# Performance work log

Measured on AMD Instinct MI355X. Metric: run time of the kernel, lower is better.

The kernel has to match this reference:

```python
import jax, jax.numpy as jnp
import numpy as np

B, N, C, H = 16, 577, 768, 12
KEEP_RATE = 0.7


def setup_inputs() -> dict:
    key = jax.random.key(0)
    k1, k2, k3 = jax.random.split(key, 3)
    x = jax.random.normal(k1, (B, N, C), dtype=jnp.float32)
    W_qkv = jax.random.normal(k2, (C, 3 * C), dtype=jnp.float32) * 0.02
    W_proj = jax.random.normal(k3, (C, C), dtype=jnp.float32) * 0.02
    b_proj = jnp.zeros((C,), dtype=jnp.float32)
    return {"x": x, "W_qkv": W_qkv, "W_proj": W_proj, "b_proj": b_proj}


def reference(x, W_qkv, W_proj, b_proj):
    b, n, c = x.shape
    h = H
    dh = c // h
    scale = dh ** (-0.5)

    # qkv projection -> q,k,v each [B,H,N,dh]
    qkv = (x @ W_qkv).reshape(b, n, 3, h, dh)
    qkv = jnp.transpose(qkv, (2, 0, 3, 1, 4))
    q, k, v = qkv[0], qkv[1], qkv[2]

    # full attention scores [B,H,N,N] (materialized, as in the source)
    attn = jnp.einsum('bhnd,bhmd->bhnm', q, k) * scale

    # --- top_pool from row-0 (CLS) scores, attn_method == 'SUM_ABS_1' ---
    # attn[:, :, 0, :] -> [B,H,N]; sum |.| over heads -> [B,N] (== mean over C=1 channel)
    attn_weight = jnp.sum(jnp.abs(attn[:, :, 0, :]), axis=1)  # [B,N]
    # exclude_first=True: drop CLS, topk over remaining N-1, alpha1=1, alpha2=0 (C==1 -> std=0)
    w = attn_weight[:, 1:]                       # [B, N-1]
    keep_num = max(int((n - 1) * KEEP_RATE), 1)  # static
    _, idx = jax.lax.top_k(w, keep_num)          # [B, keep_num]
    idx = jnp.sort(idx, axis=1)
    idx = jnp.concatenate(
        [jnp.zeros((b, 1), dtype=idx.dtype), idx + 1], axis=1)  # prepend CLS index 0
    # expand to [B, keep_num+1, dim] as in torch (pool dim kwarg == self.dim)
    keep_index = jnp.broadcast_to(idx[:, :, None], (b, keep_num + 1, c))

    # standard attention output
    a = jax.nn.softmax(attn, axis=-1)
    out = jnp.einsum('bhnm,bhmd->bhnd', a, v)    # [B,H,N,dh]
    out = jnp.transpose(out, (0, 2, 1, 3)).reshape(b, n, c)
    out = out @ W_proj + b_proj
    return out, keep_index
```

## Files before the change

### kernel.cpp

```cpp
#include <hip/hip_runtime.h>
#include <hip/hip_bf16.h>
#include <stdint.h>

#define B_    16
#define N_    577
#define C_    768
#define H_    12
#define M_    (B_*N_)
#define QKVN  (3*C_)
#define NKEEP 403
#define KROWS (NKEEP+1)
#define VTLD  640
#define PTLD  72

typedef short s16x8 __attribute__((ext_vector_type(8)));
typedef float f32x4 __attribute__((ext_vector_type(4)));

__device__ __forceinline__ unsigned short f2bf(float x){
  unsigned int u = __float_as_uint(x);
  u += 0x7FFF + ((u >> 16) & 1);
  return (unsigned short)(u >> 16);
}

__device__ __forceinline__ void gld_lds16(const void* g, void* l){
  __builtin_amdgcn_global_load_lds(
      (const __attribute__((address_space(1))) unsigned int*)g,
      (__attribute__((address_space(3))) unsigned int*)l, 16, 0, 0);
}

template<int NT, int M9, int MTILES>
__device__ __forceinline__ void tile_map(int L, int& mt, int& nt){
  constexpr int NB = MTILES*NT;
  int x = L & 7, j = L >> 3;
  if(j < M9*NT){
    nt = j/M9; mt = x*M9 + (j - nt*M9);
  } else {
    int offt = 0;
    #pragma unroll
    for(int y=0;y<8;y++) if(y<x) offt += ((NB-1-y)>>3) + 1 - M9*NT;
    int ft = offt + (j - M9*NT);
    mt = 8*M9 + ft/NT;
    nt = ft - (ft/NT)*NT;
  }
}

__global__ void k_cvt_x(const float* __restrict__ x, unsigned short* __restrict__ xb){
  int i = blockIdx.x*256 + threadIdx.x;
  float4 v = ((const float4*)x)[i];
  ushort4 o; o.x=f2bf(v.x); o.y=f2bf(v.y); o.z=f2bf(v.z); o.w=f2bf(v.w);
  ((ushort4*)xb)[i] = o;
}

__global__ void k_transpose_cvt(const float* __restrict__ in, unsigned short* __restrict__ out,
                                int R, int CC){
  __shared__ float tile[64][65];
  int r0 = blockIdx.y*64, c0 = blockIdx.x*64;
  int tx = threadIdx.x & 63, ty = threadIdx.x >> 6;
  #pragma unroll
  for(int i=0;i<16;i++){
    int r = ty + i*4;
    tile[r][tx] = in[(size_t)(r0+r)*CC + c0 + tx];
  }
  __syncthreads();
  #pragma unroll
  for(int i=0;i<16;i++){
    int c = ty + i*4;
    out[(size_t)(c0+c)*R + r0 + tx] = f2bf(tile[tx][c]);
  }
}

template<int LDC_, bool BF16OUT, bool FUSEV, int NT>
__global__ __launch_bounds__(256) void k_gemm_bt(const unsigned short* __restrict__ A,
                          const unsigned short* __restrict__ Bt,
                          void* __restrict__ Cout,
                          const float* __restrict__ bias, int Mdim,
                          unsigned short* __restrict__ vtbuf){
  __shared__ __align__(16) unsigned short As[128*32];
  __shared__ __align__(16) unsigned short Bs[128*32];
  const int t = threadIdx.x;
  const int w = t>>6, l = t&63, lq = l>>4, lr = l&15;
  const int wm = w>>1, wn = w&1;
  int mt, nt; tile_map<NT, 9, 73>(blockIdx.x, mt, nt);
  const int m0 = mt*128, n0 = nt*128;
  int rA0 = m0 + (t>>2);       if(rA0 >= Mdim) rA0 = Mdim-1;
  int rA1 = m0 + ((t+256)>>2); if(rA1 >= Mdim) rA1 = Mdim-1;
  const unsigned short* gA0 = A  + (size_t)rA0*768 + (t&3)*8;
  const unsigned short* gA1 = A  + (size_t)rA1*768 + (t&3)*8;
  const unsigned short* gB0 = Bt + (size_t)(n0 + (t>>2))*768 + (t&3)*8;
  const unsigned short* gB1 = Bt + (size_t)(n0 + ((t+256)>>2))*768 + (t&3)*8;
  unsigned short* lA0 = As + (size_t)w*512;
  unsigned short* lA1 = As + 2048 + (size_t)w*512;
  unsigned short* lB0 = Bs + (size_t)w*512;
  unsigned short* lB1 = Bs + 2048 + (size_t)w*512;
  f32x4 acc[4][4] = {};
  for(int kt=0; kt<24; ++kt){
    const int ko = kt*32;
    __syncthreads();
    gld_lds16(gA0 + ko, lA0); gld_lds16(gA1 + ko, lA1);
    gld_lds16(gB0 + ko, lB0); gld_lds16(gB1 + ko, lB1);
    __syncthreads();
    s16x8 af[4], bfr[4];
    #pragma unroll
    for(int it=0;it<4;it++) af[it]  = *(const s16x8*)&As[(wm*64+it*16+lr)*32 + lq*8];
    #pragma unroll
    for(int jt=0;jt<4;jt++) bfr[jt] = *(const s16x8*)&Bs[(wn*64+jt*16+lr)*32 + lq*8];
    #pragma unroll
    for(int it=0;it<4;it++)
      #pragma unroll
      for(int jt=0;jt<4;jt++)
        acc[it][jt] = __builtin_amdgcn_mfma_f32_16x16x32_bf16(af[it], bfr[jt], acc[it][jt], 0,0,0);
  }
  if(FUSEV && n0 >= 1536){
    #pragma unroll
    for(int it=0;it<4;it++){
      int tok0 = m0 + wm*64 + it*16 + lq*4;
      #pragma unroll
      for(int jt=0;jt<4;jt++){
        int vrow = (n0 - 1536) + wn*64 + jt*16 + lr;
        ushort4 pk; unsigned short* pks = (unsigned short*)&pk;
        #pragma unroll
        for(int r=0;r<4;r++) pks[r] = f2bf(acc[it][jt][r]);
        int b0 = tok0/577, t0 = tok0 - b0*577;
        if(tok0 + 3 < M_ && t0 + 3 < 577){
          *(ushort4*)&vtbuf[(size_t)(b0*768 + vrow)*VTLD + t0] = pk;
        } else {
          #pragma unroll
          for(int r=0;r<4;r++){
            int tg = tok0 + r;
            if(tg < M_){
              int bb = tg/577, tt = tg - bb*577;
              vtbuf[(size_t)(bb*768 + vrow)*VTLD + tt] = pks[r];
            }
          }
        }
      }
    }
  } else {
    #pragma unroll
    for(int it=0;it<4;it++){
      #pragma unroll
      for(int r=0;r<4;r++){
        int row = m0 + wm*64 + it*16 + lq*4 + r;
        if(row < Mdim){
          #pragma unroll
          for(int jt=0;jt<4;jt++){
            int col = n0 + wn*64 + jt*16 + lr;
            float v = acc[it][jt][r];
            if constexpr (BF16OUT)
              ((unsigned short*)Cout)[(size_t)row*LDC_ + col] = f2bf(v);
            else
              ((float*)Cout)[(size_t)row*LDC_ + col] = v + bias[col];
          }
        }
      }
    }
  }
}

__global__ __launch_bounds__(256) void k_gemm_bt64(const unsigned short* __restrict__ A,
                          const unsigned short* __restrict__ Bt,
                          float* __restrict__ Cout,
                          const float* __restrict__ bias, int Mdim){
  __shared__ __align__(16) unsigned short As[64*32];
  __shared__ __align__(16) unsigned short Bs[128*32];
  const int t = threadIdx.x;
  const int w = t>>6, l = t&63, lq = l>>4, lr = l&15;
  const int wm = w>>1, wn = w&1;
  int mt, nt; tile_map<6, 18, 145>(blockIdx.x, mt, nt);
  const int m0 = mt*64, n0 = nt*128;
  int rA0 = m0 + (t>>2);       if(rA0 >= Mdim) rA0 = Mdim-1;
  const unsigned short* gA0 = A  + (size_t)rA0*768 + (t&3)*8;
  const unsigned short* gB0 = Bt + (size_t)(n0 + (t>>2))*768 + (t&3)*8;
  const unsigned short* gB1 = Bt + (size_t)(n0 + ((t+256)>>2))*768 + (t&3)*8;
  unsigned short* lA0 = As + (size_t)w*512;
  unsigned short* lB0 = Bs + (size_t)w*512;
  unsigned short* lB1 = Bs + 2048 + (size_t)w*512;
  f32x4 acc[2][4] = {};
  for(int kt=0; kt<24; ++kt){
    const int ko = kt*32;
    __syncthreads();
    gld_lds16(gA0 + ko, lA0);
    gld_lds16(gB0 + ko, lB0); gld_lds16(gB1 + ko, lB1);
    __syncthreads();
    s16x8 af[2], bfr[4];
    #pragma unroll
    for(int it=0;it<2;it++) af[it]  = *(const s16x8*)&As[(wm*32+it*16+lr)*32 + lq*8];
    #pragma unroll
    for(int jt=0;jt<4;jt++) bfr[jt] = *(const s16x8*)&Bs[(wn*64+jt*16+lr)*32 + lq*8];
    #pragma unroll
    for(int it=0;it<2;it++)
      #pragma unroll
      for(int jt=0;jt<4;jt++)
        acc[it][jt] = __builtin_amdgcn_mfma_f32_16x16x32_bf16(af[it], bfr[jt], acc[it][jt], 0,0,0);
  }
  #pragma unroll
  for(int it=0;it<2;it++){
    #pragma unroll
    for(int r=0;r<4;r++){
      int row = m0 + wm*32 + it*16 + lq*4 + r;
      if(row < Mdim){
        #pragma unroll
        for(int jt=0;jt<4;jt++){
          int col = n0 + wn*64 + jt*16 + lr;
          Cout[(size_t)row*768 + col] = acc[it][jt][r] + bias[col];
        }
      }
    }
  }
}

__global__ __launch_bounds__(256,4) void k_attn(const unsigned short* __restrict__ qkv,
                                                const unsigned short* __restrict__ vtbuf,
                                                unsigned short* __restrict__ aout){
  __shared__ __align__(16) unsigned short Ks[64*64];
  __shared__ __align__(16) unsigned short Vt[64*64];
  __shared__ __align__(16) unsigned short Ptt[128*PTLD];
  __shared__ float Ls[4][2][16][4];
  const int blk = blockIdx.x;
  const int bh = blk % 192, qt = blk / 192;
  const int b = bh / 12, h = bh % 12;
  const int t = threadIdx.x, w = t>>6, l = t&63, lq = l>>4, lr = l&15;
  const size_t base = (size_t)(b*577)*2304 + h*64;
  const int q0 = qt*128;
  s16x8 bq[2][2];
  #pragma unroll
  for(int it=0;it<2;it++){
    int qrow = q0 + w*32 + it*16 + lr; if(qrow > 576) qrow = 576;
    #pragma unroll
    for(int ks=0;ks<2;ks++)
      bq[it][ks] = *(const s16x8*)&qkv[base + (size_t)qrow*2304 + ks*32 + lq*8];
  }
  const int srow = w*8 + (l>>3);
  const int cswz8 = (((l&7) ^ (l>>3)) << 3);
  unsigned short* ldsK = Ks + (size_t)w*512;
  unsigned short* ldsV = Vt + (size_t)w*512;
  const unsigned short* gVbase = vtbuf + (size_t)(bh*64)*VTLD + cswz8;

  f32x4 acc_o[2][4] = {};
  float lsum[2] = {0.f, 0.f};
  const float CEXP = 0.18033688011112043f;

  auto tile_body = [&](int j0, bool edge){
    __syncthreads();
    #pragma unroll
    for(int i=0;i<2;i++){
      int krow = j0 + i*32 + srow; if(krow > 576) krow = 576;
      gld_lds16(qkv + base + 768 + (size_t)krow*2304 + cswz8, ldsK + i*2048);
      gld_lds16(gVbase + (size_t)(i*32 + srow)*VTLD + j0,     ldsV + i*2048);
    }
    __syncthreads();
    f32x4 accs[2][4] = {};
    #pragma unroll
    for(int ks=0;ks<2;ks++){
      s16x8 ak[4];
      #pragma unroll
      for(int jt=0;jt<4;jt++){
        int j = jt*16 + lr;
        ak[jt] = *(const s16x8*)&Ks[j*64 + (((4*ks+lq) ^ (j&7))<<3)];
      }
      #pragma unroll
      for(int it=0;it<2;it++)
        #pragma unroll
        for(int jt=0;jt<4;jt++)
          accs[it][jt] = __builtin_amdgcn_mfma_f32_16x16x32_bf16(ak[jt], bq[it][ks], accs[it][jt], 0,0,0);
    }
    #pragma unroll
    for(int it=0;it<2;it++){
      int qlocal = w*32 + it*16 + lr;
      #pragma unroll
      for(int jt=0;jt<4;jt++){
        ushort4 pk;
        unsigned short* pks = (unsigned short*)&pk;
        #pragma unroll
        for(int r=0;r<4;r++){
          float p = exp2f(accs[it][jt][r] * CEXP);
          if(edge){ if(j0 + jt*16 + lq*4 + r > 576) p = 0.f; }
          lsum[it] += p;
          pks[r] = f2bf(p);
        }
        *(ushort4*)&Ptt[qlocal*PTLD + jt*16 + lq*4] = pk;
      }
    }
    #pragma unroll
    for(int ks=0;ks<2;ks++){
      s16x8 ap[2], bv[4];
      #pragma unroll
      for(int it=0;it<2;it++)
        ap[it] = *(const s16x8*)&Ptt[(w*32+it*16+lr)*PTLD + ks*32 + lq*8];
      #pragma unroll
      for(int dt=0;dt<4;dt++){
        int d = dt*16 + lr;
        bv[dt] = *(const s16x8*)&Vt[d*64 + (((4*ks+lq) ^ (d&7))<<3)];
      }
      #pragma unroll
      for(int it=0;it<2;it++)
        #pragma unroll
        for(int dt=0;dt<4;dt++)
          acc_o[it][dt] = __builtin_amdgcn_mfma_f32_16x16x32_bf16(ap[it], bv[dt], acc_o[it][dt], 0,0,0);
    }
  };
  for(int j0=0; j0<576; j0+=64) tile_body(j0, false);
  tile_body(576, true);

  #pragma unroll
  for(int it=0;it<2;it++) Ls[w][it][lr][lq] = lsum[it];
  #pragma unroll
  for(int it=0;it<2;it++){
    #pragma unroll
    for(int r=0;r<4;r++){
      int n = q0 + w*32 + it*16 + lq*4 + r;
      if(n <= 576){
        int q16 = lq*4 + r;
        float lt = Ls[w][it][q16][0] + Ls[w][it][q16][1] + Ls[w][it][q16][2] + Ls[w][it][q16][3];
        float inv = 1.f / lt;
        #pragma unroll
        for(int dt=0;dt<4;dt++)
          aout[(size_t)(b*577+n)*768 + h*64 + dt*16 + lr] = f2bf(acc_o[it][dt][r]*inv);
      }
    }
  }
}

__global__ void k_qcls(const float* __restrict__ x, const float* __restrict__ Wqkv,
                       float* __restrict__ qcls){
  __shared__ float xs[768];
  __shared__ float part[4][64];
  const int b = blockIdx.y, j0 = blockIdx.x*64;
  const int t = threadIdx.x;
  const float* xr = x + (size_t)b*577*768;
  xs[t] = xr[t]; xs[t+256] = xr[t+256]; xs[t+512] = xr[t+512];
  __syncthreads();
  const int jl = t & 63, cs = t >> 6;
  float acc = 0.f;
  const float* wp = Wqkv + (size_t)(cs*192)*2304 + j0 + jl;
  #pragma unroll 4
  for(int c=0;c<192;c++){ acc += xs[cs*192+c] * wp[0]; wp += 2304; }
  part[cs][jl] = acc;
  __syncthreads();
  if(t < 64) qcls[b*768 + j0 + t] = part[0][t]+part[1][t]+part[2][t]+part[3][t];
}
__global__ void k_u(const float* __restrict__ Wqkv, const float* __restrict__ qcls,
                    float* __restrict__ u){
  int h = blockIdx.x, b = blockIdx.y, c = threadIdx.x;
  const float* qc = qcls + b*768 + h*64;
  const float* wr = Wqkv + (size_t)c*2304 + 768 + h*64;
  float acc = 0.f;
  #pragma unroll
  for(int d=0;d<64;d++) acc += wr[d]*qc[d];
  u[(size_t)(b*12+h)*768 + c] = acc;
}
__global__ void k_attw(const float* __restrict__ x, const float* __restrict__ u,
                       float* __restrict__ attw){
  int blk = blockIdx.x;
  int b = blk/577, m = blk%577;
  int lane = threadIdx.x;
  const float* xr = x + (size_t)(b*577+m)*768;
  const float* ub = u + (size_t)b*12*768;
  float part[12];
  #pragma unroll
  for(int h=0;h<12;h++) part[h]=0.f;
  #pragma unroll
  for(int i=0;i<12;i++){
    float xv = xr[i*64 + lane];
    #pragma unroll
    for(int h=0;h<12;h++) part[h] += xv * ub[h*768 + i*64 + lane];
  }
  float s = 0.f;
  #pragma unroll
  for(int h=0;h<12;h++){
    float v = part[h];
    #pragma unroll
    for(int off=32; off; off>>=1) v += __shfl_xor(v, off);
    s += fabsf(v);
  }
  if(lane==0) attw[b*577 + m] = 0.125f * s;
}
__global__ void k_topk(const float* __restrict__ attw, int* __restrict__ idxbuf){
  __shared__ float sw[576];
  __shared__ int wtot[9];
  int b = blockIdx.x, t = threadIdx.x;
  float wv = attw[b*577 + 1 + t];
  sw[t] = wv;
  __syncthreads();
  int rank = 0;
  for(int j=0;j<576;j++){
    float wj = sw[j];
    rank += (wj > wv) || (wj == wv && j < t);
  }
  bool kept = rank < NKEEP;
  unsigned long long mask = __ballot(kept);
  int wid = t>>6, lane = t&63;
  int pos = __popcll(mask & ((1ull<<lane)-1ull));
  if(lane==0) wtot[wid] = __popcll(mask);
  __syncthreads();
  int off0 = 0;
  for(int q=0;q<wid;q++) off0 += wtot[q];
  if(kept) idxbuf[b*KROWS + 1 + off0 + pos] = t+1;
  if(t==0) idxbuf[b*KROWS] = 0;
}
__global__ void k_fill_keep(const int* __restrict__ idxbuf, float* __restrict__ out2){
  int i4 = blockIdx.x*256 + threadIdx.x;
  float v = (float)idxbuf[i4/192];
  ((float4*)out2)[i4] = make_float4(v,v,v,v);
}

extern "C" void kernel_launch(void* const* d_in, const int* in_sizes, int n_in,
                              void* d_out, int out_size, void* d_ws, size_t ws_size,
                              hipStream_t stream){
  const float* x     = (const float*)d_in[0];
  const float* Wqkv  = (const float*)d_in[1];
  const float* Wproj = (const float*)d_in[2];
  const float* bias  = (const float*)d_in[3];
  float* out  = (float*)d_out;
  float* out2 = out + (size_t)M_*768;

  char* ws = (char*)d_ws;
  size_t off = 0;
  auto alloc = [&](size_t bytes)->void*{ void* p = ws + off; off += (bytes + 255) & ~(size_t)255; return p; };
  unsigned short* xb     = (unsigned short*)alloc((size_t)M_*768*2);
  unsigned short* wqkvT  = (unsigned short*)alloc((size_t)QKVN*768*2);
  unsigned short* wprojT = (unsigned short*)alloc((size_t)768*768*2);
  unsigned short* qkvb   = (unsigned short*)alloc((size_t)M_*QKVN*2);
  unsigned short* aoutb  = (unsigned short*)alloc((size_t)M_*768*2);
  unsigned short* vtbuf  = (unsigned short*)alloc((size_t)192*64*VTLD*2);
  float* qcls   = (float*)alloc((size_t)16*768*4);
  float* u      = (float*)alloc((size_t)16*12*768*4);
  float* attw   = (float*)alloc((size_t)16*577*4);
  int*   idxbuf = (int*)alloc((size_t)16*KROWS*4);

  k_cvt_x<<<6924, 256, 0, stream>>>(x, xb);
  k_transpose_cvt<<<dim3(36,12), 256, 0, stream>>>(Wqkv,  wqkvT, 768, 2304);
  k_transpose_cvt<<<dim3(12,12), 256, 0, stream>>>(Wproj, wprojT, 768, 768);
  k_gemm_bt<QKVN, true, true, 18><<<73*18, 256, 0, stream>>>(xb, wqkvT, qkvb, nullptr, M_, vtbuf);
  k_qcls<<<dim3(12,16), 256, 0, stream>>>(x, Wqkv, qcls);
  k_u<<<dim3(12,16), 768, 0, stream>>>(Wqkv, qcls, u);
  k_attw<<<16*577, 64, 0, stream>>>(x, u, attw);
  k_topk<<<16, 576, 0, stream>>>(attw, idxbuf);
  k_fill_keep<<<(16*KROWS*768/4 + 255)/256, 256, 0, stream>>>(idxbuf, out2);
  k_attn<<<960, 256, 0, stream>>>(qkvb, vtbuf, aoutb);
  k_gemm_bt64<<<145*6, 256, 0, stream>>>(aoutb, wprojT, out, bias, M_);
}
```

Before: 282.8 us.

## Rewrite QKV GEMM as 256x256 tile with pipelined LDS double buffering

```diff
diff --git a/kernel.cpp b/kernel.cpp
--- a/kernel.cpp
+++ b/kernel.cpp
@@ -69,59 +69,135 @@
   }
 }
 
-template<int LDC_, bool BF16OUT, bool FUSEV, int NT>
-__global__ __launch_bounds__(256) void k_gemm_bt(const unsigned short* __restrict__ A,
+__global__ __launch_bounds__(512,2) void k_gemm_qkv(const unsigned short* __restrict__ A,
                           const unsigned short* __restrict__ Bt,
-                          void* __restrict__ Cout,
-                          const float* __restrict__ bias, int Mdim,
+                          unsigned short* __restrict__ qkvb,
                           unsigned short* __restrict__ vtbuf){
-  __shared__ __align__(16) unsigned short As[128*32];
-  __shared__ __align__(16) unsigned short Bs[128*32];
+  __shared__ __align__(16) unsigned short L[8][8192];
   const int t = threadIdx.x;
   const int w = t>>6, l = t&63, lq = l>>4, lr = l&15;
-  const int wm = w>>1, wn = w&1;
-  int mt, nt; tile_map<NT, 9, 73>(blockIdx.x, mt, nt);
-  const int m0 = mt*128, n0 = nt*128;
-  int rA0 = m0 + (t>>2);       if(rA0 >= Mdim) rA0 = Mdim-1;
-  int rA1 = m0 + ((t+256)>>2); if(rA1 >= Mdim) rA1 = Mdim-1;
-  const unsigned short* gA0 = A  + (size_t)rA0*768 + (t&3)*8;
-  const unsigned short* gA1 = A  + (size_t)rA1*768 + (t&3)*8;
-  const unsigned short* gB0 = Bt + (size_t)(n0 + (t>>2))*768 + (t&3)*8;
-  const unsigned short* gB1 = Bt + (size_t)(n0 + ((t+256)>>2))*768 + (t&3)*8;
-  unsigned short* lA0 = As + (size_t)w*512;
-  unsigned short* lA1 = As + 2048 + (size_t)w*512;
-  unsigned short* lB0 = Bs + (size_t)w*512;
-  unsigned short* lB1 = Bs + 2048 + (size_t)w*512;
-  f32x4 acc[4][4] = {};
-  for(int kt=0; kt<24; ++kt){
-    const int ko = kt*32;
-    __syncthreads();
-    gld_lds16(gA0 + ko, lA0); gld_lds16(gA1 + ko, lA1);
-    gld_lds16(gB0 + ko, lB0); gld_lds16(gB1 + ko, lB1);
-    __syncthreads();
-    s16x8 af[4], bfr[4];
-    #pragma unroll
-    for(int it=0;it<4;it++) af[it]  = *(const s16x8*)&As[(wm*64+it*16+lr)*32 + lq*8];
-    #pragma unroll
-    for(int jt=0;jt<4;jt++) bfr[jt] = *(const s16x8*)&Bs[(wn*64+jt*16+lr)*32 + lq*8];
-    #pragma unroll
-    for(int it=0;it<4;it++)
-      #pragma unroll
-      for(int jt=0;jt<4;jt++)
-        acc[it][jt] = __builtin_amdgcn_mfma_f32_16x16x32_bf16(af[it], bfr[jt], acc[it][jt], 0,0,0);
-  }
-  if(FUSEV && n0 >= 1536){
-    #pragma unroll
-    for(int it=0;it<4;it++){
-      int tok0 = m0 + wm*64 + it*16 + lq*4;
-      #pragma unroll
-      for(int jt=0;jt<4;jt++){
-        int vrow = (n0 - 1536) + wn*64 + jt*16 + lr;
+  const int wm = w>>2, wn = w&3;
+
+  int orig = blockIdx.x;
+  int xid = orig & 7, j = orig >> 3;
+  int wgid = (xid < 5 ? xid*42 : 210 + (xid-5)*41) + j;
+  int mt = wgid/9, nt = wgid - mt*9;
+  const int m0 = mt*256, n0 = nt*256;
+
+  const int rr = w*8 + (l>>3);
+  const int csw = ((l&7)*8) ^ ((l&32)?16:0);
+  int ra0 = m0 + rr;        if(ra0 >= M_) ra0 = M_-1;
+  int ra1 = m0 + 64 + rr;   if(ra1 >= M_) ra1 = M_-1;
+  int ra2 = m0 + 128 + rr;  if(ra2 >= M_) ra2 = M_-1;
+  int ra3 = m0 + 192 + rr;  if(ra3 >= M_) ra3 = M_-1;
+  const unsigned short* pA00 = A + (size_t)ra0*768 + csw;
+  const unsigned short* pA01 = A + (size_t)ra1*768 + csw;
+  const unsigned short* pA10 = A + (size_t)ra2*768 + csw;
+  const unsigned short* pA11 = A + (size_t)ra3*768 + csw;
+  const unsigned short* pB00 = Bt + (size_t)(n0 + rr)*768 + csw;
+  const unsigned short* pB01 = Bt + (size_t)(n0 + 64 + rr)*768 + csw;
+  const unsigned short* pB10 = Bt + (size_t)(n0 + 128 + rr)*768 + csw;
+  const unsigned short* pB11 = Bt + (size_t)(n0 + 192 + rr)*768 + csw;
+
+#define STAGE_A(H, KT, SLT) do{ \
+  unsigned short* d_ = &L[((H)<<1)|(SLT)][(w*8)<<6]; \
+  gld_lds16(pA##H##0 + (size_t)(KT)*64, d_); \
+  gld_lds16(pA##H##1 + (size_t)(KT)*64, d_ + 4096); \
+}while(0)
+#define STAGE_B(H, KT, SLT) do{ \
+  unsigned short* d_ = &L[4 + (((H)<<1)|(SLT))][(w*8)<<6]; \
+  gld_lds16(pB##H##0 + (size_t)(KT)*64, d_); \
+  gld_lds16(pB##H##1 + (size_t)(KT)*64, d_ + 4096); \
+}while(0)
+#define READ_A(MH) do{ \
+  _Pragma("unroll") \
+  for(int mf=0; mf<4; mf++){ \
+    const int R_ = (MH)*64 + mf*16 + lr; \
+    const int rx_ = (R_&4)<<2; \
+    af[mf][0] = *(const s16x8*)&baseA[R_*64 + ((lq*8) ^ rx_)]; \
+    af[mf][1] = *(const s16x8*)&baseA[R_*64 + ((32 + lq*8) ^ rx_)]; \
+  } \
+}while(0)
+#define READ_B() do{ \
+  _Pragma("unroll") \
+  for(int nf=0; nf<4; nf++){ \
+    const int R_ = (wn&1)*64 + nf*16 + lr; \
+    const int rx_ = (R_&4)<<2; \
+    bf[nf][0] = *(const s16x8*)&baseB[R_*64 + ((lq*8) ^ rx_)]; \
+    bf[nf][1] = *(const s16x8*)&baseB[R_*64 + ((32 + lq*8) ^ rx_)]; \
+  } \
+}while(0)
+#define MMA_Q(MH, NH) do{ \
+  __builtin_amdgcn_s_setprio(1); \
+  _Pragma("unroll") \
+  for(int ks=0; ks<2; ks++){ \
+    _Pragma("unroll") \
+    for(int mf=0; mf<4; mf++){ \
+      _Pragma("unroll") \
+      for(int nf=0; nf<2; nf++){ \
+        acc[(MH)*4+mf][(NH)*2+nf] = __builtin_amdgcn_mfma_f32_16x16x32_bf16( \
+            af[mf][ks], bf[(NH)*2+nf][ks], acc[(MH)*4+mf][(NH)*2+nf], 0,0,0); \
+      } } } \
+  __builtin_amdgcn_s_setprio(0); \
+}while(0)
+
+  f32x4 acc[8][4] = {};
+  s16x8 af[4][2], bf[4][2];
+  const unsigned short* baseA0 = &L[wm<<1][0];
+  const unsigned short* baseB0 = &L[4 + ((wn>>1)<<1)][0];
+
+  STAGE_A(0, 0, 0); STAGE_A(1, 0, 0); STAGE_B(0, 0, 0); STAGE_B(1, 0, 0);
+  STAGE_B(0, 1, 1); STAGE_B(1, 1, 1); STAGE_A(0, 1, 1);
+  asm volatile("s_waitcnt vmcnt(6)" ::: "memory");
+  __builtin_amdgcn_s_barrier();
+
+  for(int g=0; g<12; ++g){
+    const int s = g&1;
+    const unsigned short* baseA = baseA0 + (s<<13);
+    const unsigned short* baseB = baseB0 + (s<<13);
+    READ_A(0);
+    READ_B();
+    if(g<11){ STAGE_A(1, g+1, s^1); }
+    __builtin_amdgcn_s_barrier();
+    asm volatile("s_waitcnt lgkmcnt(0)" ::: "memory");
+    __builtin_amdgcn_sched_barrier(0);
+    MMA_Q(0,0);
+    __builtin_amdgcn_s_barrier();
+    if(g<10){ STAGE_B(0, g+2, s); }
+    __builtin_amdgcn_s_barrier();
+    MMA_Q(0,1);
+    __builtin_amdgcn_s_barrier();
+    READ_A(1);
+    if(g<10){ STAGE_B(1, g+2, s); }
+    __builtin_amdgcn_s_barrier();
+    asm volatile("s_waitcnt lgkmcnt(0)" ::: "memory");
+    __builtin_amdgcn_sched_barrier(0);
+    MMA_Q(1,1);
+    __builtin_amdgcn_s_barrier();
+    if(g<10){
+      STAGE_A(0, g+2, s);
+      asm volatile("s_waitcnt vmcnt(6)" ::: "memory");
+    } else if(g==10){
+      asm volatile("s_waitcnt vmcnt(0)" ::: "memory");
+    }
+    __builtin_amdgcn_s_barrier();
+    MMA_Q(1,0);
+    __builtin_amdgcn_s_barrier();
+  }
+
+  if(n0 >= 1536){
+    #pragma unroll
+    for(int mi=0; mi<8; mi++){
+      int tok0 = m0 + wm*128 + mi*16 + lq*4;
+      int b0 = tok0/577, t0 = tok0 - b0*577;
+      bool fast = (tok0 + 3 < M_) && (t0 + 3 < 577);
+      #pragma unroll
+      for(int ni=0; ni<4; ni++){
+        int vrow = (n0 - 1536) + wn*64 + ni*16 + lr;
         ushort4 pk; unsigned short* pks = (unsigned short*)&pk;
         #pragma unroll
-        for(int r=0;r<4;r++) pks[r] = f2bf(acc[it][jt][r]);
-        int b0 = tok0/577, t0 = tok0 - b0*577;
-        if(tok0 + 3 < M_ && t0 + 3 < 577){
+        for(int r=0;r<4;r++) pks[r] = f2bf(acc[mi][ni][r]);
+        if(fast){
           *(ushort4*)&vtbuf[(size_t)(b0*768 + vrow)*VTLD + t0] = pk;
         } else {
           #pragma unroll
@@ -137,24 +213,25 @@
     }
   } else {
     #pragma unroll
-    for(int it=0;it<4;it++){
+    for(int mi=0; mi<8; mi++){
       #pragma unroll
       for(int r=0;r<4;r++){
-        int row = m0 + wm*64 + it*16 + lq*4 + r;
-        if(row < Mdim){
+        int row = m0 + wm*128 + mi*16 + lq*4 + r;
+        if(row < M_){
           #pragma unroll
-          for(int jt=0;jt<4;jt++){
-            int col = n0 + wn*64 + jt*16 + lr;
-            float v = acc[it][jt][r];
-            if constexpr (BF16OUT)
-              ((unsigned short*)Cout)[(size_t)row*LDC_ + col] = f2bf(v);
-            else
-              ((float*)Cout)[(size_t)row*LDC_ + col] = v + bias[col];
+          for(int ni=0; ni<4; ni++){
+            int col = n0 + wn*64 + ni*16 + lr;
+            qkvb[(size_t)row*2304 + col] = f2bf(acc[mi][ni][r]);
           }
         }
       }
     }
   }
+#undef STAGE_A
+#undef STAGE_B
+#undef READ_A
+#undef READ_B
+#undef MMA_Q
 }
 
 __global__ __launch_bounds__(256) void k_gemm_bt64(const unsigned short* __restrict__ A,
@@ -431,7 +508,7 @@
   k_cvt_x<<<6924, 256, 0, stream>>>(x, xb);
   k_transpose_cvt<<<dim3(36,12), 256, 0, stream>>>(Wqkv,  wqkvT, 768, 2304);
   k_transpose_cvt<<<dim3(12,12), 256, 0, stream>>>(Wproj, wprojT, 768, 768);
-  k_gemm_bt<QKVN, true, true, 18><<<73*18, 256, 0, stream>>>(xb, wqkvT, qkvb, nullptr, M_, vtbuf);
+  k_gemm_qkv<<<333, 512, 0, stream>>>(xb, wqkvT, qkvb, vtbuf);
   k_qcls<<<dim3(12,16), 256, 0, stream>>>(x, Wqkv, qcls);
   k_u<<<dim3(12,16), 768, 0, stream>>>(Wqkv, qcls, u);
   k_attw<<<16*577, 64, 0, stream>>>(x, u, attw);
```

Measured after the change: 295.3 us. +4.4%, slower.

## Double-buffer QKV GEMM with swizzled LDS, BK=64 and async prefetch

Applied to the files above, without the earlier changes.

```diff
diff --git a/kernel.cpp b/kernel.cpp
--- a/kernel.cpp
+++ b/kernel.cpp
@@ -69,48 +69,91 @@
   }
 }
 
-template<int LDC_, bool BF16OUT, bool FUSEV, int NT>
-__global__ __launch_bounds__(256) void k_gemm_bt(const unsigned short* __restrict__ A,
+__global__ __launch_bounds__(256,2) void k_gemm_qkv(const unsigned short* __restrict__ A,
                           const unsigned short* __restrict__ Bt,
-                          void* __restrict__ Cout,
-                          const float* __restrict__ bias, int Mdim,
+                          unsigned short* __restrict__ qkvb,
                           unsigned short* __restrict__ vtbuf){
-  __shared__ __align__(16) unsigned short As[128*32];
-  __shared__ __align__(16) unsigned short Bs[128*32];
+  __shared__ __align__(16) unsigned short L[4][8192];
   const int t = threadIdx.x;
   const int w = t>>6, l = t&63, lq = l>>4, lr = l&15;
   const int wm = w>>1, wn = w&1;
-  int mt, nt; tile_map<NT, 9, 73>(blockIdx.x, mt, nt);
+  int mt, nt; tile_map<18, 9, 73>(blockIdx.x, mt, nt);
   const int m0 = mt*128, n0 = nt*128;
-  int rA0 = m0 + (t>>2);       if(rA0 >= Mdim) rA0 = Mdim-1;
-  int rA1 = m0 + ((t+256)>>2); if(rA1 >= Mdim) rA1 = Mdim-1;
-  const unsigned short* gA0 = A  + (size_t)rA0*768 + (t&3)*8;
-  const unsigned short* gA1 = A  + (size_t)rA1*768 + (t&3)*8;
-  const unsigned short* gB0 = Bt + (size_t)(n0 + (t>>2))*768 + (t&3)*8;
-  const unsigned short* gB1 = Bt + (size_t)(n0 + ((t+256)>>2))*768 + (t&3)*8;
-  unsigned short* lA0 = As + (size_t)w*512;
-  unsigned short* lA1 = As + 2048 + (size_t)w*512;
-  unsigned short* lB0 = Bs + (size_t)w*512;
-  unsigned short* lB1 = Bs + 2048 + (size_t)w*512;
+
+  const int rr = w*8 + (l>>3);
+  const int csw = ((l&7)<<3) ^ ((((l>>3)&1)<<5) | (((l>>4)&3)<<3));
+  const unsigned short* pA[4];
+  const unsigned short* pB[4];
+  #pragma unroll
+  for(int i=0;i<4;i++){
+    int ra = m0 + rr + 32*i; if(ra >= M_) ra = M_-1;
+    pA[i] = A  + (size_t)ra*768 + csw;
+    pB[i] = Bt + (size_t)(n0 + rr + 32*i)*768 + csw;
+  }
+  const int fswz = ((lr&1)<<5) | (((lr>>1)&3)<<3);
+
+#define STAGE(KT, SLT) do{ \
+  unsigned short* dA_ = &L[(SLT)][w*512]; \
+  unsigned short* dB_ = &L[2+(SLT)][w*512]; \
+  _Pragma("unroll") \
+  for(int i_=0;i_<4;i_++){ \
+    gld_lds16(pA[i_] + (size_t)(KT)*64, dA_ + i_*2048); \
+    gld_lds16(pB[i_] + (size_t)(KT)*64, dB_ + i_*2048); \
+  } \
+}while(0)
+#define READ_ALL(S) do{ \
+  const unsigned short* bA_ = &L[(S)][0]; \
+  const unsigned short* bB_ = &L[2+(S)][0]; \
+  _Pragma("unroll") \
+  for(int mf=0;mf<4;mf++){ \
+    const int R_ = wm*64 + mf*16 + lr; \
+    af[mf][0] = *(const s16x8*)&bA_[R_*64 + ((lq*8) ^ fswz)]; \
+    af[mf][1] = *(const s16x8*)&bA_[R_*64 + ((32 + lq*8) ^ fswz)]; \
+  } \
+  _Pragma("unroll") \
+  for(int nf=0;nf<4;nf++){ \
+    const int R_ = wn*64 + nf*16 + lr; \
+    bf[nf][0] = *(const s16x8*)&bB_[R_*64 + ((lq*8) ^ fswz)]; \
+    bf[nf][1] = *(const s16x8*)&bB_[R_*64 + ((32 + lq*8) ^ fswz)]; \
+  } \
+}while(0)
+#define MMA_ALL() do{ \
+  __builtin_amdgcn_s_setprio(1); \
+  _Pragma("unroll") \
+  for(int ks=0;ks<2;ks++) \
+    _Pragma("unroll") \
+    for(int mf=0;mf<4;mf++) \
+      _Pragma("unroll") \
+      for(int nf=0;nf<4;nf++) \
+        acc[mf][nf] = __builtin_amdgcn_mfma_f32_16x16x32_bf16(af[mf][ks], bf[nf][ks], acc[mf][nf], 0,0,0); \
+  __builtin_amdgcn_s_setprio(0); \
+}while(0)
+
   f32x4 acc[4][4] = {};
-  for(int kt=0; kt<24; ++kt){
-    const int ko = kt*32;
-    __syncthreads();
-    gld_lds16(gA0 + ko, lA0); gld_lds16(gA1 + ko, lA1);
-    gld_lds16(gB0 + ko, lB0); gld_lds16(gB1 + ko, lB1);
-    __syncthreads();
-    s16x8 af[4], bfr[4];
-    #pragma unroll
-    for(int it=0;it<4;it++) af[it]  = *(const s16x8*)&As[(wm*64+it*16+lr)*32 + lq*8];
-    #pragma unroll
-    for(int jt=0;jt<4;jt++) bfr[jt] = *(const s16x8*)&Bs[(wn*64+jt*16+lr)*32 + lq*8];
-    #pragma unroll
-    for(int it=0;it<4;it++)
-      #pragma unroll
-      for(int jt=0;jt<4;jt++)
-        acc[it][jt] = __builtin_amdgcn_mfma_f32_16x16x32_bf16(af[it], bfr[jt], acc[it][jt], 0,0,0);
-  }
-  if(FUSEV && n0 >= 1536){
+  s16x8 af[4][2], bf[4][2];
+
+  STAGE(0, 0);
+  STAGE(1, 1);
+  asm volatile("s_waitcnt vmcnt(8)" ::: "memory");
+  __builtin_amdgcn_s_barrier();
+
+  for(int g=0; g<12; ++g){
+    const int s = g&1;
+    READ_ALL(s);
+    asm volatile("s_waitcnt lgkmcnt(0)" ::: "memory");
+    __builtin_amdgcn_sched_barrier(0);
+    __builtin_amdgcn_s_barrier();
+    if(g<10){ STAGE(g+2, s); }
+    MMA_ALL();
+    if(g<10){
+      asm volatile("s_waitcnt vmcnt(8)" ::: "memory");
+    } else if(g==10){
+      asm volatile("s_waitcnt vmcnt(0)" ::: "memory");
+    }
+    __builtin_amdgcn_s_barrier();
+  }
+
+  if(n0 >= 1536){
     #pragma unroll
     for(int it=0;it<4;it++){
       int tok0 = m0 + wm*64 + it*16 + lq*4;
@@ -141,20 +184,19 @@
       #pragma unroll
       for(int r=0;r<4;r++){
         int row = m0 + wm*64 + it*16 + lq*4 + r;
-        if(row < Mdim){
+        if(row < M_){
           #pragma unroll
           for(int jt=0;jt<4;jt++){
             int col = n0 + wn*64 + jt*16 + lr;
-            float v = acc[it][jt][r];
-            if constexpr (BF16OUT)
-              ((unsigned short*)Cout)[(size_t)row*LDC_ + col] = f2bf(v);
-            else
-              ((float*)Cout)[(size_t)row*LDC_ + col] = v + bias[col];
+            qkvb[(size_t)row*2304 + col] = f2bf(acc[it][jt][r]);
           }
         }
       }
     }
   }
+#undef STAGE
+#undef READ_ALL
+#undef MMA_ALL
 }
 
 __global__ __launch_bounds__(256) void k_gemm_bt64(const unsigned short* __restrict__ A,
@@ -431,7 +473,7 @@
   k_cvt_x<<<6924, 256, 0, stream>>>(x, xb);
   k_transpose_cvt<<<dim3(36,12), 256, 0, stream>>>(Wqkv,  wqkvT, 768, 2304);
   k_transpose_cvt<<<dim3(12,12), 256, 0, stream>>>(Wproj, wprojT, 768, 768);
-  k_gemm_bt<QKVN, true, true, 18><<<73*18, 256, 0, stream>>>(xb, wqkvT, qkvb, nullptr, M_, vtbuf);
+  k_gemm_qkv<<<73*18, 256, 0, stream>>>(xb, wqkvT, qkvb, vtbuf);
   k_qcls<<<dim3(12,16), 256, 0, stream>>>(x, Wqkv, qcls);
   k_u<<<dim3(12,16), 768, 0, stream>>>(Wqkv, qcls, u);
   k_attw<<<16*577, 64, 0, stream>>>(x, u, attw);
```

Result: faster. 276.2 us (-2.4%).

## Load QKV GEMM fragments directly from global into registers with double buffering

Applied to the files above, without the earlier changes.

```diff
diff --git a/kernel.cpp b/kernel.cpp
--- a/kernel.cpp
+++ b/kernel.cpp
@@ -69,48 +69,58 @@
   }
 }
 
-template<int LDC_, bool BF16OUT, bool FUSEV, int NT>
-__global__ __launch_bounds__(256) void k_gemm_bt(const unsigned short* __restrict__ A,
+__global__ __launch_bounds__(256) void k_gemm_qkv(const unsigned short* __restrict__ A,
                           const unsigned short* __restrict__ Bt,
-                          void* __restrict__ Cout,
-                          const float* __restrict__ bias, int Mdim,
+                          unsigned short* __restrict__ qkvb,
                           unsigned short* __restrict__ vtbuf){
-  __shared__ __align__(16) unsigned short As[128*32];
-  __shared__ __align__(16) unsigned short Bs[128*32];
   const int t = threadIdx.x;
   const int w = t>>6, l = t&63, lq = l>>4, lr = l&15;
   const int wm = w>>1, wn = w&1;
-  int mt, nt; tile_map<NT, 9, 73>(blockIdx.x, mt, nt);
+  int mt, nt; tile_map<18, 9, 73>(blockIdx.x, mt, nt);
   const int m0 = mt*128, n0 = nt*128;
-  int rA0 = m0 + (t>>2);       if(rA0 >= Mdim) rA0 = Mdim-1;
-  int rA1 = m0 + ((t+256)>>2); if(rA1 >= Mdim) rA1 = Mdim-1;
-  const unsigned short* gA0 = A  + (size_t)rA0*768 + (t&3)*8;
-  const unsigned short* gA1 = A  + (size_t)rA1*768 + (t&3)*8;
-  const unsigned short* gB0 = Bt + (size_t)(n0 + (t>>2))*768 + (t&3)*8;
-  const unsigned short* gB1 = Bt + (size_t)(n0 + ((t+256)>>2))*768 + (t&3)*8;
-  unsigned short* lA0 = As + (size_t)w*512;
-  unsigned short* lA1 = As + 2048 + (size_t)w*512;
-  unsigned short* lB0 = Bs + (size_t)w*512;
-  unsigned short* lB1 = Bs + 2048 + (size_t)w*512;
+
+  const unsigned short* pA[4];
+  const unsigned short* pB[4];
+  #pragma unroll
+  for(int mf=0;mf<4;mf++){
+    int ra = m0 + wm*64 + mf*16 + lr; if(ra >= M_) ra = M_-1;
+    pA[mf] = A + (size_t)ra*768 + lq*8;
+  }
+  #pragma unroll
+  for(int nf=0;nf<4;nf++){
+    pB[nf] = Bt + (size_t)(n0 + wn*64 + nf*16 + lr)*768 + lq*8;
+  }
+
   f32x4 acc[4][4] = {};
-  for(int kt=0; kt<24; ++kt){
-    const int ko = kt*32;
-    __syncthreads();
-    gld_lds16(gA0 + ko, lA0); gld_lds16(gA1 + ko, lA1);
-    gld_lds16(gB0 + ko, lB0); gld_lds16(gB1 + ko, lB1);
-    __syncthreads();
-    s16x8 af[4], bfr[4];
-    #pragma unroll
-    for(int it=0;it<4;it++) af[it]  = *(const s16x8*)&As[(wm*64+it*16+lr)*32 + lq*8];
-    #pragma unroll
-    for(int jt=0;jt<4;jt++) bfr[jt] = *(const s16x8*)&Bs[(wn*64+jt*16+lr)*32 + lq*8];
-    #pragma unroll
-    for(int it=0;it<4;it++)
-      #pragma unroll
-      for(int jt=0;jt<4;jt++)
-        acc[it][jt] = __builtin_amdgcn_mfma_f32_16x16x32_bf16(af[it], bfr[jt], acc[it][jt], 0,0,0);
-  }
-  if(FUSEV && n0 >= 1536){
+  s16x8 aX[4], bX[4], aY[4], bY[4];
+
+#define MMA_ALL(AR, BR) do{ \
+  _Pragma("unroll") \
+  for(int mf_=0;mf_<4;mf_++) \
+    _Pragma("unroll") \
+    for(int nf_=0;nf_<4;nf_++) \
+      acc[mf_][nf_] = __builtin_amdgcn_mfma_f32_16x16x32_bf16(AR[mf_], BR[nf_], acc[mf_][nf_], 0,0,0); \
+}while(0)
+
+  #pragma unroll
+  for(int i=0;i<4;i++){ aX[i] = *(const s16x8*)(pA[i]); bX[i] = *(const s16x8*)(pB[i]); }
+
+  for(int kp=0; kp<11; ++kp){
+    #pragma unroll
+    for(int i=0;i<4;i++){ aY[i] = *(const s16x8*)(pA[i]+32); bY[i] = *(const s16x8*)(pB[i]+32); }
+    MMA_ALL(aX, bX);
+    #pragma unroll
+    for(int i=0;i<4;i++){ aX[i] = *(const s16x8*)(pA[i]+64); bX[i] = *(const s16x8*)(pB[i]+64);
+                          pA[i] += 64; pB[i] += 64; }
+    MMA_ALL(aY, bY);
+  }
+  #pragma unroll
+  for(int i=0;i<4;i++){ aY[i] = *(const s16x8*)(pA[i]+32); bY[i] = *(const s16x8*)(pB[i]+32); }
+  MMA_ALL(aX, bX);
+  MMA_ALL(aY, bY);
+#undef MMA_ALL
+
+  if(n0 >= 1536){
     #pragma unroll
     for(int it=0;it<4;it++){
       int tok0 = m0 + wm*64 + it*16 + lq*4;
@@ -141,15 +151,11 @@
       #pragma unroll
       for(int r=0;r<4;r++){
         int row = m0 + wm*64 + it*16 + lq*4 + r;
-        if(row < Mdim){
+        if(row < M_){
           #pragma unroll
           for(int jt=0;jt<4;jt++){
             int col = n0 + wn*64 + jt*16 + lr;
-            float v = acc[it][jt][r];
-            if constexpr (BF16OUT)
-              ((unsigned short*)Cout)[(size_t)row*LDC_ + col] = f2bf(v);
-            else
-              ((float*)Cout)[(size_t)row*LDC_ + col] = v + bias[col];
+            qkvb[(size_t)row*2304 + col] = f2bf(acc[it][jt][r]);
           }
         }
       }
@@ -431,7 +437,7 @@
   k_cvt_x<<<6924, 256, 0, stream>>>(x, xb);
   k_transpose_cvt<<<dim3(36,12), 256, 0, stream>>>(Wqkv,  wqkvT, 768, 2304);
   k_transpose_cvt<<<dim3(12,12), 256, 0, stream>>>(Wproj, wprojT, 768, 768);
-  k_gemm_bt<QKVN, true, true, 18><<<73*18, 256, 0, stream>>>(xb, wqkvT, qkvb, nullptr, M_, vtbuf);
+  k_gemm_qkv<<<73*18, 256, 0, stream>>>(xb, wqkvT, qkvb, vtbuf);
   k_qcls<<<dim3(12,16), 256, 0, stream>>>(x, Wqkv, qcls);
   k_u<<<dim3(12,16), 768, 0, stream>>>(Wqkv, qcls, u);
   k_attw<<<16*577, 64, 0, stream>>>(x, u, attw);
```

Measured after the change: 368.4 us. 30.3% more time.
